# Kernel tuning notes

Hardware: AMD Instinct MI355X
Metric: run time of the kernel (lower is better)

Reference implementation:

```python
import jax, jax.numpy as jnp
import numpy as np

N_NODES = 100000
N_EDGES = 3200000
B = 64            # number of graphs / RNA batch
DIM = 16          # GINE hidden dim
NFP = 33          # protein node feature dim
EMB = 128         # embedding dim
MAXLEN = 3000     # rna_global length (conv1d in_channels)
LOCLEN = 2998     # rna_local length = 3000 - log4(64) + 1
NF = 32           # n_filters
KS = 8            # conv kernel size -> 128-8+1 = 121
FC_IN = NF * 121  # 3872
BN_EPS = 1e-5


def setup_inputs() -> dict:
    key = jax.random.key(0)
    ks = jax.random.split(key, 32)
    s = 0.1
    p = {}
    # forward data args
    p['pro_x'] = jax.random.normal(ks[0], (N_NODES, NFP), jnp.float32)
    p['pro_edge_index'] = jax.random.randint(ks[1], (2, N_EDGES), 0, N_NODES, jnp.int32)
    p['pro_weight'] = jax.random.uniform(ks[2], (N_EDGES, 1), jnp.float32)
    p['pro_batch'] = jnp.sort(jax.random.randint(ks[3], (N_NODES,), 0, B, jnp.int32))
    p['rna_global'] = jax.random.randint(ks[4], (B, MAXLEN), 0, 5, jnp.int32)
    p['rna_local'] = jax.random.randint(ks[5], (B, LOCLEN), 0, 65, jnp.int32)
    # GINE layer 1 (33 -> 16)
    p['g1_w1'] = jax.random.normal(ks[6], (NFP, DIM), jnp.float32) * s
    p['g1_b1'] = jnp.zeros((DIM,), jnp.float32)
    p['g1_w2'] = jax.random.normal(ks[7], (DIM, DIM), jnp.float32) * s
    p['g1_b2'] = jnp.zeros((DIM,), jnp.float32)
    p['g1_ew'] = jax.random.normal(ks[8], (1, NFP), jnp.float32) * s  # edge Linear(1, 33)
    p['g1_eb'] = jnp.zeros((NFP,), jnp.float32)
    p['g1_eps'] = jnp.zeros((), jnp.float32)
    # GINE layers 2-5 (16 -> 16), stacked on leading axis
    p['g_w1'] = jax.random.normal(ks[9], (4, DIM, DIM), jnp.float32) * s
    p['g_b1'] = jnp.zeros((4, DIM), jnp.float32)
    p['g_w2'] = jax.random.normal(ks[10], (4, DIM, DIM), jnp.float32) * s
    p['g_b2'] = jnp.zeros((4, DIM), jnp.float32)
    p['g_ew'] = jax.random.normal(ks[11], (4, 1, DIM), jnp.float32) * s  # edge Linear(1, 16)
    p['g_eb'] = jnp.zeros((4, DIM), jnp.float32)
    p['g_eps'] = jnp.zeros((4,), jnp.float32)
    # BatchNorm1d x5
    p['bn_gamma'] = jnp.ones((5, DIM), jnp.float32)
    p['bn_beta'] = jnp.zeros((5, DIM), jnp.float32)
    # fc1_xp (16 -> 128)
    p['fc1_xp_w'] = jax.random.normal(ks[12], (DIM, EMB), jnp.float32) * s
    p['fc1_xp_b'] = jnp.zeros((EMB,), jnp.float32)
    # RNA branch
    p['emb1'] = jax.random.normal(ks[13], (5, EMB), jnp.float32)
    p['emb2'] = jax.random.normal(ks[14], (65, EMB), jnp.float32)
    p['convr1_w'] = jax.random.normal(ks[15], (NF, MAXLEN, KS), jnp.float32) * 0.01
    p['convr1_b'] = jnp.zeros((NF,), jnp.float32)
    p['convr2_w'] = jax.random.normal(ks[16], (NF, LOCLEN, KS), jnp.float32) * 0.01
    p['convr2_b'] = jnp.zeros((NF,), jnp.float32)
    p['fcxr_w'] = jax.random.normal(ks[17], (FC_IN, EMB), jnp.float32) * 0.01
    p['fcxr_b'] = jnp.zeros((EMB,), jnp.float32)
    return p


def _gine(x, src, dst, ew, w1, b1, w2, b2, ew_w, ew_b, eps):
    # GINEConv: out = MLP((1+eps)*x + sum_j relu(x_j + edge_lin(e_ij)))
    e = ew @ ew_w + ew_b                       # [E, d]
    m = jax.nn.relu(x[src] + e)                # [E, d] gather + fuse
    agg = jax.ops.segment_sum(m, dst, num_segments=N_NODES)
    h = (1.0 + eps) * x + agg
    return jax.nn.relu(h @ w1 + b1) @ w2 + b2


def _bn(x, gamma, beta):
    mu = jnp.mean(x, axis=0)
    var = jnp.var(x, axis=0)
    return (x - mu) * jax.lax.rsqrt(var + BN_EPS) * gamma + beta


def _rna_branch(tokens, emb, cw, cb, fcw, fcb):
    x = emb[tokens]                            # [B, L, 128]
    y = jax.lax.conv_general_dilated(x, cw, (1,), 'VALID',
                                     dimension_numbers=('NCH', 'OIH', 'NCH'))
    y = y + cb[None, :, None]                  # [B, 32, 121]
    return y.reshape(y.shape[0], -1) @ fcw + fcb


def reference(pro_x, pro_edge_index, pro_weight, pro_batch, rna_global, rna_local,
              g1_w1, g1_b1, g1_w2, g1_b2, g1_ew, g1_eb, g1_eps,
              g_w1, g_b1, g_w2, g_b2, g_ew, g_eb, g_eps,
              bn_gamma, bn_beta, fc1_xp_w, fc1_xp_b,
              emb1, emb2, convr1_w, convr1_b, convr2_w, convr2_b, fcxr_w, fcxr_b):
    src, dst = pro_edge_index[0], pro_edge_index[1]
    # RNA global / local branches (shared fc_xr)
    xrg = _rna_branch(rna_global, emb1, convr1_w, convr1_b, fcxr_w, fcxr_b)
    xrl = _rna_branch(rna_local, emb2, convr2_w, convr2_b, fcxr_w, fcxr_b)
    # protein GINE stack
    xp = jax.nn.relu(_gine(pro_x, src, dst, pro_weight,
                           g1_w1, g1_b1, g1_w2, g1_b2, g1_ew, g1_eb, g1_eps))
    xp = _bn(xp, bn_gamma[0], bn_beta[0])
    for i in range(4):
        xp = jax.nn.relu(_gine(xp, src, dst, pro_weight,
                               g_w1[i], g_b1[i], g_w2[i], g_b2[i],
                               g_ew[i], g_eb[i], g_eps[i]))
        xp = _bn(xp, bn_gamma[i + 1], bn_beta[i + 1])
    # global mean pool over graphs
    sums = jax.ops.segment_sum(xp, pro_batch, num_segments=B)
    cnt = jax.ops.segment_sum(jnp.ones((N_NODES, 1), xp.dtype), pro_batch, num_segments=B)
    xp = jax.nn.relu((sums / jnp.maximum(cnt, 1.0)) @ fc1_xp_w + fc1_xp_b)
    # dropout in eval mode -> identity
    xc_rna = 0.5 * (xrg + xrl)
    return (xc_rna, xp)
```

## Files before the change

### kernel.cpp

```cpp
#include <hip/hip_runtime.h>
#include <hip/hip_fp16.h>

#define N_NODES 100000
#define N_EDGES 3200000
#define BGR 64
#define DIM 16
#define NFP 33
#define ROW1 32
#define H1STR 36
#define EMB 128
#define MAXLEN 3000
#define LOCLEN 2998
#define NF 32
#define KS 8
#define OUTT 121
#define FC_IN 3872
#define BN_EPSV 1e-5f
#define POOL_CHUNK 256
#define POOL_BLKS 391
#define MLPB 391
#define AGGB 3125
#define NBIN 391
#define BCNT_BLK 512
#define P1_CHUNK 4096
#define P1_BLOCKS 782
#define MAXBIN 9088
#define NKC 32
#define KCH 121
#define WDEC (1.f / 32767.f)

__global__ void __launch_bounds__(256) k_bincnt(const int* __restrict__ dst,
                                                int* __restrict__ bh) {
    __shared__ int hist[NBIN];
    int t = threadIdx.x, bid = blockIdx.x;
    for (int b = t; b < NBIN; b += 256) hist[b] = 0;
    __syncthreads();
    int e0 = bid * (N_EDGES / BCNT_BLK);
    int e1 = e0 + (N_EDGES / BCNT_BLK);
    for (int e = e0 + t; e < e1; e += 256) atomicAdd(&hist[dst[e] >> 8], 1);
    __syncthreads();
    for (int b = t; b < NBIN; b += 256) bh[b * BCNT_BLK + bid] = hist[b];
}

__global__ void __launch_bounds__(512) k_binscan(const int* __restrict__ bh,
                                                 int* __restrict__ binoff,
                                                 int* __restrict__ bincur) {
    __shared__ int sc[512];
    int t = threadIdx.x;
    int s = 0;
    if (t < NBIN) {
        const int* row = bh + t * BCNT_BLK;
        for (int k = 0; k < BCNT_BLK; k++) s += row[k];
    }
    sc[t] = s;
    __syncthreads();
    for (int off = 1; off < 512; off <<= 1) {
        int v = (t >= off) ? sc[t - off] : 0;
        __syncthreads();
        sc[t] += v;
        __syncthreads();
    }
    int excl = sc[t] - s;
    if (t <= NBIN) binoff[t] = excl;
    if (t < NBIN) bincur[t] = excl;
}

__global__ void __launch_bounds__(256) k_part1(const int* __restrict__ src,
                                               const int* __restrict__ dst,
                                               const float* __restrict__ w,
                                               int* __restrict__ bincur,
                                               int2* __restrict__ tmp_sw) {
    __shared__ int2 srec[P1_CHUNK];
    __shared__ unsigned short sbin[P1_CHUNK];
    __shared__ unsigned short sperm[P1_CHUNK];
    __shared__ int hist[NBIN];
    __shared__ int off[NBIN];
    __shared__ int cur[NBIN];
    __shared__ int base[NBIN];
    __shared__ int sc[512];
    int t = threadIdx.x;
    int g0 = blockIdx.x * P1_CHUNK;
    int cn = N_EDGES - g0; if (cn > P1_CHUNK) cn = P1_CHUNK;
    for (int b = t; b < NBIN; b += 256) hist[b] = 0;
    __syncthreads();
    for (int j = t; j < cn; j += 256) {
        int d = dst[g0 + j];
        int b = d >> 8;
        sbin[j] = (unsigned short)b;
        srec[j] = make_int2(src[g0 + j] | ((d & 255) << 20), __float_as_int(w[g0 + j]));
        atomicAdd(&hist[b], 1);
    }
    __syncthreads();
    sc[t] = (t < NBIN) ? hist[t] : 0;
    sc[256 + t] = (256 + t < NBIN) ? hist[256 + t] : 0;
    __syncthreads();
    for (int o = 1; o <= 256; o <<= 1) {
        int v0 = (t >= o) ? sc[t - o] : 0;
        int v1 = sc[256 + t - o];
        __syncthreads();
        sc[t] += v0;
        sc[256 + t] += v1;
        __syncthreads();
    }
    for (int b = t; b < NBIN; b += 256) {
        int e = sc[b] - hist[b];
        off[b] = e;
        cur[b] = e;
        int c = hist[b];
        base[b] = c ? atomicAdd(&bincur[b], c) : 0;
    }
    __syncthreads();
    for (int j = t; j < cn; j += 256) {
        int p = atomicAdd(&cur[sbin[j]], 1);
        sperm[p] = (unsigned short)j;
    }
    __syncthreads();
    for (int p = t; p < cn; p += 256) {
        int j = sperm[p];
        int b = sbin[j];
        tmp_sw[base[b] + (p - off[b])] = srec[j];
    }
}

__global__ void __launch_bounds__(256) k_part2(const int2* __restrict__ tmp_sw,
                                               const int* __restrict__ binoff,
                                               unsigned* __restrict__ er,
                                               int* __restrict__ ptr) {
    __shared__ unsigned char sdl[MAXBIN];
    __shared__ unsigned short perm[MAXBIN];
    __shared__ int hist[256];
    __shared__ int cur[256];
    __shared__ int sc[256];
    int t = threadIdx.x, b = blockIdx.x;
    int nlo = b << 8;
    int e0 = binoff[b], e1 = binoff[b + 1];
    int cnt = e1 - e0;
    int stage = cnt < MAXBIN ? cnt : MAXBIN;
    hist[t] = 0;
    __syncthreads();
    for (int j = t; j < stage; j += 256) {
        unsigned char dl = (unsigned char)((tmp_sw[e0 + j].x >> 20) & 255);
        sdl[j] = dl;
        atomicAdd(&hist[dl], 1);
    }
    for (int j = stage + t; j < cnt; j += 256)
        atomicAdd(&hist[(tmp_sw[e0 + j].x >> 20) & 255], 1);
    __syncthreads();
    int v = hist[t];
    sc[t] = v;
    __syncthreads();
    for (int off = 1; off < 256; off <<= 1) {
        int u = (t >= off) ? sc[t - off] : 0;
        __syncthreads();
        sc[t] += u;
        __syncthreads();
    }
    int excl = sc[t] - v;
    cur[t] = excl;
    if (nlo + t < N_NODES) ptr[nlo + t] = e0 + excl;
    if (b == NBIN - 1 && t == 0) ptr[N_NODES] = N_EDGES;
    __syncthreads();
    for (int j = t; j < stage; j += 256) {
        int p = atomicAdd(&cur[sdl[j]], 1);
        perm[p] = (unsigned short)j;
    }
    __syncthreads();
    for (int j = stage + t; j < cnt; j += 256) {
        int2 sw = tmp_sw[e0 + j];
        int p = atomicAdd(&cur[(sw.x >> 20) & 255], 1);
        unsigned wq = (unsigned)(__int_as_float(sw.y) * 32767.f + 0.5f);
        er[e0 + p] = ((unsigned)sw.x & 0x1FFFFu) | (wq << 17);
    }
    for (int p = t; p < stage; p += 256) {
        int2 sw = tmp_sw[e0 + perm[p]];
        unsigned wq = (unsigned)(__int_as_float(sw.y) * 32767.f + 0.5f);
        er[e0 + p] = ((unsigned)sw.x & 0x1FFFFu) | (wq << 17);
    }
}

__global__ void k_half1(const float* __restrict__ x, __half* __restrict__ xh,
                        __half* __restrict__ xh32) {
    int i = blockIdx.x * blockDim.x + threadIdx.x;
    if (i < N_NODES * NFP) {
        int n = i / NFP, f = i - n * NFP;
        __half v = __float2half(x[i]);
        if (f < 32) xh[n * ROW1 + f] = v;
        else xh32[n] = v;
    }
}

__device__ __forceinline__ void acc8p(float a[8], uint4 r, float wv,
                                      const float* __restrict__ ewf,
                                      const float* __restrict__ ebf) {
    float2 f01 = __half22float2(*(__half2*)&r.x);
    float2 f23 = __half22float2(*(__half2*)&r.y);
    float2 f45 = __half22float2(*(__half2*)&r.z);
    float2 f67 = __half22float2(*(__half2*)&r.w);
    float x[8] = {f01.x, f01.y, f23.x, f23.y, f45.x, f45.y, f67.x, f67.y};
    #pragma unroll
    for (int j = 0; j < 8; j++)
        a[j] += fmaxf(x[j] + fmaf(wv, ewf[j], ebf[j]), 0.f);
}

__device__ __forceinline__ void acc8s(float a[8], uint4 r, float wv,
                                      const float* __restrict__ scf,
                                      const float* __restrict__ cbf,
                                      const float* __restrict__ ewf) {
    float2 f01 = __half22float2(*(__half2*)&r.x);
    float2 f23 = __half22float2(*(__half2*)&r.y);
    float2 f45 = __half22float2(*(__half2*)&r.z);
    float2 f67 = __half22float2(*(__half2*)&r.w);
    float x[8] = {f01.x, f01.y, f23.x, f23.y, f45.x, f45.y, f67.x, f67.y};
    #pragma unroll
    for (int j = 0; j < 8; j++)
        a[j] += fmaxf(fmaf(x[j], scf[j], fmaf(wv, ewf[j], cbf[j])), 0.f);
}

__global__ void __launch_bounds__(256) k_agg1(
    const __half* __restrict__ xh, const __half* __restrict__ xh32,
    const int* __restrict__ ptr, const unsigned* __restrict__ er,
    const float* __restrict__ ew, const float* __restrict__ ebv,
    const float* __restrict__ epsp, float* __restrict__ h) {
    int t = threadIdx.x;
    int wave = t >> 6, lane = t & 63;
    int nl = lane >> 3;
    int slot = (lane >> 2) & 1;
    int q = lane & 3;
    float ewf[8], ebf[8];
    #pragma unroll
    for (int j = 0; j < 8; j++) { ewf[j] = ew[q * 8 + j]; ebf[j] = ebv[q * 8 + j]; }
    float ew32 = ew[32], eb32 = ebv[32];
    float ep = 1.f + epsp[0];
    int node = blockIdx.x * 32 + wave * 8 + nl;
    int e0 = ptr[node], e1 = ptr[node + 1];
    float a[8] = {0, 0, 0, 0, 0, 0, 0, 0};
    float a32 = 0.f;
    int i = e0 + slot;
    while (i + 2 < e1) {
        unsigned ev0 = er[i];
        unsigned ev1 = er[i + 2];
        int s0 = ev0 & 0x1FFFF, s1 = ev1 & 0x1FFFF;
        float wv0 = (float)(ev0 >> 17) * WDEC;
        float wv1 = (float)(ev1 >> 17) * WDEC;
        uint4 r0 = *(const uint4*)(xh + s0 * ROW1 + q * 8);
        uint4 r1 = *(const uint4*)(xh + s1 * ROW1 + q * 8);
        acc8p(a, r0, wv0, ewf, ebf);
        acc8p(a, r1, wv1, ewf, ebf);
        if (q == 0) {
            a32 += fmaxf(__half2float(xh32[s0]) + fmaf(wv0, ew32, eb32), 0.f);
            a32 += fmaxf(__half2float(xh32[s1]) + fmaf(wv1, ew32, eb32), 0.f);
        }
        i += 4;
    }
    if (i < e1) {
        unsigned ev = er[i];
        int s = ev & 0x1FFFF;
        float wv = (float)(ev >> 17) * WDEC;
        uint4 r = *(const uint4*)(xh + s * ROW1 + q * 8);
        acc8p(a, r, wv, ewf, ebf);
        if (q == 0)
            a32 += fmaxf(__half2float(xh32[s]) + fmaf(wv, ew32, eb32), 0.f);
    }
    #pragma unroll
    for (int j = 0; j < 8; j++) a[j] += __shfl_xor(a[j], 4);
    a32 += __shfl_xor(a32, 4);
    if (slot == 0) {
        uint4 sraw = *(const uint4*)(xh + node * ROW1 + q * 8);
        float2 s01 = __half22float2(*(__half2*)&sraw.x);
        float2 s23 = __half22float2(*(__half2*)&sraw.y);
        float2 s45 = __half22float2(*(__half2*)&sraw.z);
        float2 s67 = __half22float2(*(__half2*)&sraw.w);
        float* hp = h + node * H1STR + q * 8;
        *(float4*)hp = make_float4(ep * s01.x + a[0], ep * s01.y + a[1],
                                   ep * s23.x + a[2], ep * s23.y + a[3]);
        *(float4*)(hp + 4) = make_float4(ep * s45.x + a[4], ep * s45.y + a[5],
                                         ep * s67.x + a[6], ep * s67.y + a[7]);
        if (q == 0)
            h[node * H1STR + 32] = ep * __half2float(xh32[node]) + a32;
    }
}

__global__ void __launch_bounds__(256) k_agg16(
    const __half* __restrict__ zh, const int* __restrict__ ptr,
    const unsigned* __restrict__ er,
    const float* __restrict__ ew, const float* __restrict__ ebv,
    const float* __restrict__ epsp,
    const float* __restrict__ bnstat, const float* __restrict__ gamma,
    const float* __restrict__ beta, float* __restrict__ h) {
    int t = threadIdx.x;
    int wave = t >> 6, lane = t & 63;
    int nl = lane >> 3;
    int slot = (lane >> 1) & 3;
    int hh = lane & 1;
    float ep = 1.f + epsp[0];
    const float invn = 1.f / (float)N_NODES;
    float scf[8], shf[8], cbf[8], ewf[8];
    #pragma unroll
    for (int j = 0; j < 8; j++) {
        int f = hh * 8 + j;
        float mu = bnstat[f] * invn;
        float var = bnstat[DIM + f] * invn - mu * mu;
        float sc = gamma[f] * rsqrtf(var + BN_EPSV);
        scf[j] = sc;
        shf[j] = beta[f] - mu * sc;
        cbf[j] = shf[j] + ebv[f];
        ewf[j] = ew[f];
    }
    int node = blockIdx.x * 32 + wave * 8 + nl;
    int e0 = ptr[node], e1 = ptr[node + 1];
    float a[8] = {0, 0, 0, 0, 0, 0, 0, 0};
    int i = e0 + slot;
    while (i + 4 < e1) {
        unsigned ev0 = er[i];
        unsigned ev1 = er[i + 4];
        float wv0 = (float)(ev0 >> 17) * WDEC;
        float wv1 = (float)(ev1 >> 17) * WDEC;
        uint4 r0 = *(const uint4*)(zh + (ev0 & 0x1FFFFu) * DIM + hh * 8);
        uint4 r1 = *(const uint4*)(zh + (ev1 & 0x1FFFFu) * DIM + hh * 8);
        acc8s(a, r0, wv0, scf, cbf, ewf);
        acc8s(a, r1, wv1, scf, cbf, ewf);
        i += 8;
    }
    if (i < e1) {
        unsigned ev = er[i];
        float wv = (float)(ev >> 17) * WDEC;
        uint4 r = *(const uint4*)(zh + (ev & 0x1FFFFu) * DIM + hh * 8);
        acc8s(a, r, wv, scf, cbf, ewf);
    }
    #pragma unroll
    for (int j = 0; j < 8; j++) a[j] += __shfl_xor(a[j], 2);
    #pragma unroll
    for (int j = 0; j < 8; j++) a[j] += __shfl_xor(a[j], 4);
    if (slot == 0) {
        uint4 sraw = *(const uint4*)(zh + node * DIM + hh * 8);
        float2 s01 = __half22float2(*(__half2*)&sraw.x);
        float2 s23 = __half22float2(*(__half2*)&sraw.y);
        float2 s45 = __half22float2(*(__half2*)&sraw.z);
        float2 s67 = __half22float2(*(__half2*)&sraw.w);
        float xs[8] = {s01.x, s01.y, s23.x, s23.y, s45.x, s45.y, s67.x, s67.y};
        float o8[8];
        #pragma unroll
        for (int j = 0; j < 8; j++)
            o8[j] = ep * fmaf(xs[j], scf[j], shf[j]) + a[j];
        float* hp = h + node * DIM + hh * 8;
        *(float4*)hp = make_float4(o8[0], o8[1], o8[2], o8[3]);
        *(float4*)(hp + 4) = make_float4(o8[4], o8[5], o8[6], o8[7]);
    }
}

__device__ __forceinline__ void mlp_bn_tail(float zv[16], bool active, int t,
                                            float* __restrict__ part) {
    __shared__ float red[4][32];
    float zs[16], zq[16];
    #pragma unroll
    for (int o = 0; o < 16; o++) {
        zs[o] = active ? zv[o] : 0.f;
        zq[o] = active ? zv[o] * zv[o] : 0.f;
    }
    #pragma unroll
    for (int m = 1; m <= 32; m <<= 1) {
        #pragma unroll
        for (int o = 0; o < 16; o++) {
            zs[o] += __shfl_xor(zs[o], m);
            zq[o] += __shfl_xor(zq[o], m);
        }
    }
    int wave = t >> 6, lane = t & 63;
    if (lane == 0) {
        #pragma unroll
        for (int o = 0; o < 16; o++) {
            red[wave][o] = zs[o];
            red[wave][16 + o] = zq[o];
        }
    }
    __syncthreads();
    if (t < 32)
        part[blockIdx.x * 32 + t] = red[0][t] + red[1][t] + red[2][t] + red[3][t];
}

__device__ __forceinline__ void store_zh(__half* __restrict__ zh, int n, float zv[16]) {
    __half2 p[8];
    #pragma unroll
    for (int j = 0; j < 8; j++) p[j] = __floats2half2_rn(zv[2 * j], zv[2 * j + 1]);
    *(uint4*)(zh + n * DIM) = *(uint4*)&p[0];
    *(uint4*)(zh + n * DIM + 8) = *(uint4*)&p[4];
}

__global__ void __launch_bounds__(256) k_mlp16(
    const float* __restrict__ h,
    const float* __restrict__ W1, const float* __restrict__ b1,
    const float* __restrict__ W2, const float* __restrict__ b2,
    __half* __restrict__ zh, float* __restrict__ part) {
    __shared__ float W1s[256], W2s[256], b1s[16], b2s[16];
    int t = threadIdx.x;
    W1s[t] = W1[t];
    W2s[t] = W2[t];
    if (t < 16) { b1s[t] = b1[t]; b2s[t] = b2[t]; }
    __syncthreads();
    int n = blockIdx.x * 256 + t;
    bool active = n < N_NODES;
    float zv[16];
    if (active) {
        float hv[16];
        #pragma unroll
        for (int j = 0; j < 4; j++) {
            float4 v = *(const float4*)(h + n * DIM + j * 4);
            hv[j * 4] = v.x; hv[j * 4 + 1] = v.y; hv[j * 4 + 2] = v.z; hv[j * 4 + 3] = v.w;
        }
        float tv[16];
        #pragma unroll
        for (int o = 0; o < 16; o++) {
            float s = b1s[o];
            #pragma unroll
            for (int f = 0; f < 16; f++) s += hv[f] * W1s[f * 16 + o];
            tv[o] = fmaxf(s, 0.f);
        }
        #pragma unroll
        for (int o = 0; o < 16; o++) {
            float s = b2s[o];
            #pragma unroll
            for (int f = 0; f < 16; f++) s += tv[f] * W2s[f * 16 + o];
            zv[o] = fmaxf(s, 0.f);
        }
        store_zh(zh, n, zv);
    }
    mlp_bn_tail(zv, active, t, part);
}

__global__ void __launch_bounds__(256) k_mlp1(
    const float* __restrict__ h,
    const float* __restrict__ W1, const float* __restrict__ b1,
    const float* __restrict__ W2, const float* __restrict__ b2,
    __half* __restrict__ zh, float* __restrict__ part) {
    __shared__ float W1s[NFP * 16], W2s[256], b1s[16], b2s[16];
    int t = threadIdx.x;
    for (int j = t; j < NFP * 16; j += 256) W1s[j] = W1[j];
    W2s[t] = W2[t];
    if (t < 16) { b1s[t] = b1[t]; b2s[t] = b2[t]; }
    __syncthreads();
    int n = blockIdx.x * 256 + t;
    bool active = n < N_NODES;
    float zv[16];
    if (active) {
        float hv[NFP];
        #pragma unroll
        for (int j = 0; j < 8; j++) {
            float4 v = *(const float4*)(h + n * H1STR + j * 4);
            hv[j * 4] = v.x; hv[j * 4 + 1] = v.y; hv[j * 4 + 2] = v.z; hv[j * 4 + 3] = v.w;
        }
        hv[32] = h[n * H1STR + 32];
        float tv[16];
        #pragma unroll
        for (int o = 0; o < 16; o++) {
            float s = b1s[o];
            #pragma unroll
            for (int f = 0; f < NFP; f++) s += hv[f] * W1s[f * 16 + o];
            tv[o] = fmaxf(s, 0.f);
        }
        #pragma unroll
        for (int o = 0; o < 16; o++) {
            float s = b2s[o];
            #pragma unroll
            for (int f = 0; f < 16; f++) s += tv[f] * W2s[f * 16 + o];
            zv[o] = fmaxf(s, 0.f);
        }
        store_zh(zh, n, zv);
    }
    mlp_bn_tail(zv, active, t, part);
}

__global__ void __launch_bounds__(1024) k_bnred(const float* __restrict__ part,
                                                float* __restrict__ bnstat) {
    __shared__ float red[1024];
    int t = threadIdx.x;
    int f = t & 31, g = t >> 5;
    float s = 0.f;
    for (int i = g; i < MLPB; i += 32) s += part[i * 32 + f];
    red[t] = s;
    __syncthreads();
    for (int off = 512; off >= 32; off >>= 1) {
        if (t < off) red[t] += red[t + off];
        __syncthreads();
    }
    if (t < 32) bnstat[t] = red[t];
}

__global__ void __launch_bounds__(256) k_pool(const __half* __restrict__ zh,
                                              const int* __restrict__ batch,
                                              const float* __restrict__ bnstat,
                                              const float* __restrict__ gamma,
                                              const float* __restrict__ beta,
                                              float* __restrict__ gsum,
                                              float* __restrict__ gcnt) {
    __shared__ float lsum[BGR * DIM];
    __shared__ float lcnt[BGR];
    int t = threadIdx.x;
    for (int j = t; j < BGR * DIM; j += 256) lsum[j] = 0.f;
    if (t < BGR) lcnt[t] = 0.f;
    __syncthreads();
    int f = t & 15, r = t >> 4;
    const float invn = 1.f / (float)N_NODES;
    float mu = bnstat[f] * invn;
    float var = bnstat[DIM + f] * invn - mu * mu;
    float sc = gamma[f] * rsqrtf(var + BN_EPSV);
    float sh = beta[f] - mu * sc;
    int start = blockIdx.x * POOL_CHUNK;
    float acc = 0.f, cacc = 0.f;
    int cur = -1;
    for (int i = 0; i < POOL_CHUNK / 16; i++) {
        int n = start + r + i * 16;
        if (n >= N_NODES) break;
        int b = batch[n];
        if (b != cur) {
            if (cur >= 0) {
                atomicAdd(&lsum[cur * DIM + f], acc);
                if (f == 0) atomicAdd(&lcnt[cur], cacc);
            }
            cur = b; acc = 0.f; cacc = 0.f;
        }
        acc += fmaf(__half2float(zh[n * DIM + f]), sc, sh);
        cacc += 1.f;
    }
    if (cur >= 0) {
        atomicAdd(&lsum[cur * DIM + f], acc);
        if (f == 0) atomicAdd(&lcnt[cur], cacc);
    }
    __syncthreads();
    for (int j = t; j < BGR * DIM; j += 256) {
        float v = lsum[j];
        if (v != 0.f) atomicAdd(&gsum[j], v);
    }
    if (t < BGR) {
        float v = lcnt[t];
        if (v != 0.f) atomicAdd(&gcnt[t], v);
    }
}

__global__ void k_xp(const float* __restrict__ gsum, const float* __restrict__ gcnt,
                     const float* __restrict__ w, const float* __restrict__ bias,
                     float* __restrict__ out) {
    int b = blockIdx.x;
    int e = threadIdx.x;
    float inv = 1.f / fmaxf(gcnt[b], 1.f);
    float acc = bias[e];
    #pragma unroll
    for (int f = 0; f < DIM; f++) acc += gsum[b * DIM + f] * inv * w[f * EMB + e];
    out[b * EMB + e] = fmaxf(acc, 0.f);
}

__global__ void __launch_bounds__(256) k_bucket(const int* __restrict__ tok, int L, int V,
                                                int* __restrict__ blist,
                                                int* __restrict__ bptr) {
    __shared__ int hist[65];
    __shared__ int cursor[65];
    int b = blockIdx.x, t = threadIdx.x;
    if (t < V) hist[t] = 0;
    __syncthreads();
    for (int l = t; l < L; l += 256) atomicAdd(&hist[tok[b * L + l]], 1);
    __syncthreads();
    if (t == 0) {
        int run = 0;
        for (int v = 0; v < V; v++) {
            cursor[v] = run;
            bptr[b * (V + 1) + v] = run;
            run += hist[v];
        }
        bptr[b * (V + 1) + V] = run;
    }
    __syncthreads();
    for (int l = t; l < L; l += 256) {
        int v = tok[b * L + l];
        int p = atomicAdd(&cursor[v], 1);
        blist[b * L + p] = l;
    }
}

__global__ void __launch_bounds__(256) k_wsum(const int* __restrict__ blist,
                                              const int* __restrict__ bptr,
                                              const float* __restrict__ cw,
                                              float* __restrict__ W, int L, int V) {
    int b = blockIdx.x, v = blockIdx.y;
    int t = threadIdx.x, o = t >> 3, k = t & 7;
    int s = bptr[b * (V + 1) + v], e = bptr[b * (V + 1) + v + 1];
    __shared__ int tk[256];
    const float* cwp = cw + o * (L * KS) + k;
    float acc = 0.f;
    for (int j0 = s; j0 < e; j0 += 256) {
        int lim = e - j0; if (lim > 256) lim = 256;
        __syncthreads();
        if (t < lim) tk[t] = blist[b * L + j0 + t];
        __syncthreads();
        for (int j = 0; j < lim; j++) acc += cwp[tk[j] * KS];
    }
    W[((b * NF + o) * V + v) * KS + k] = acc;
}

__global__ void k_y(const float* __restrict__ Wg, const float* __restrict__ Wl,
                    const float* __restrict__ emb1, const float* __restrict__ emb2,
                    const float* __restrict__ cb1, const float* __restrict__ cb2,
                    float* __restrict__ yg, float* __restrict__ yl) {
    int which = blockIdx.y;
    int bo = blockIdx.x;
    int b = bo >> 5, o = bo & 31;
    int t = threadIdx.x;
    const float* W = which ? Wl : Wg;
    const float* emb = which ? emb2 : emb1;
    const float* cb = which ? cb2 : cb1;
    float* y = which ? yl : yg;
    int V = which ? 65 : 5;
    __shared__ float Wsh[65 * KS];
    const float* Wrow = W + (b * NF + o) * V * KS;
    for (int j = t; j < V * KS; j += 128) Wsh[j] = Wrow[j];
    __syncthreads();
    if (t < OUTT) {
        float acc = cb[o];
        for (int v = 0; v < V; v++) {
            const float* ep = emb + v * EMB + t;
            #pragma unroll
            for (int k = 0; k < KS; k++) acc += Wsh[v * KS + k] * ep[k];
        }
        y[(b * NF + o) * OUTT + t] = acc;
    }
}

__global__ void __launch_bounds__(128) k_fcpart(const float* __restrict__ yg,
                                                const float* __restrict__ yl,
                                                const float* __restrict__ w,
                                                float* __restrict__ partial) {
    int b = blockIdx.x, which = blockIdx.y, kc = blockIdx.z;
    const float* y = which ? yl : yg;
    int e = threadIdx.x;
    __shared__ float ych[KCH];
    int j0 = kc * KCH;
    if (e < KCH) ych[e] = y[b * FC_IN + j0 + e];
    __syncthreads();
    float acc = 0.f;
    #pragma unroll 4
    for (int jj = 0; jj < KCH; jj++) acc += ych[jj] * w[(j0 + jj) * EMB + e];
    partial[((which * BGR + b) * NKC + kc) * EMB + e] = acc;
}

__global__ void k_fcred(const float* __restrict__ partial, const float* __restrict__ bias,
                        float* __restrict__ out) {
    int b = blockIdx.x;
    int e = threadIdx.x;
    const float* pg = partial + b * NKC * EMB + e;
    const float* pl = partial + (BGR + b) * NKC * EMB + e;
    float ag = bias[e], al = bias[e];
    #pragma unroll
    for (int k = 0; k < NKC; k++) { ag += pg[k * EMB]; al += pl[k * EMB]; }
    out[b * EMB + e] = 0.5f * (ag + al);
}

extern "C" void kernel_launch(void* const* d_in, const int* in_sizes, int n_in,
                              void* d_out, int out_size, void* d_ws, size_t ws_size,
                              hipStream_t stream) {
    const float* pro_x = (const float*)d_in[0];
    const int* eidx = (const int*)d_in[1];
    const int* esrc = eidx;
    const int* edst = eidx + N_EDGES;
    const float* pw = (const float*)d_in[2];
    const int* batch = (const int*)d_in[3];
    const int* rg = (const int*)d_in[4];
    const int* rl = (const int*)d_in[5];
    const float* g1_w1 = (const float*)d_in[6];
    const float* g1_b1 = (const float*)d_in[7];
    const float* g1_w2 = (const float*)d_in[8];
    const float* g1_b2 = (const float*)d_in[9];
    const float* g1_ew = (const float*)d_in[10];
    const float* g1_eb = (const float*)d_in[11];
    const float* g1_eps = (const float*)d_in[12];
    const float* g_w1 = (const float*)d_in[13];
    const float* g_b1 = (const float*)d_in[14];
    const float* g_w2 = (const float*)d_in[15];
    const float* g_b2 = (const float*)d_in[16];
    const float* g_ew = (const float*)d_in[17];
    const float* g_eb = (const float*)d_in[18];
    const float* g_eps = (const float*)d_in[19];
    const float* bn_gamma = (const float*)d_in[20];
    const float* bn_beta = (const float*)d_in[21];
    const float* fc1_xp_w = (const float*)d_in[22];
    const float* fc1_xp_b = (const float*)d_in[23];
    const float* emb1 = (const float*)d_in[24];
    const float* emb2 = (const float*)d_in[25];
    const float* convr1_w = (const float*)d_in[26];
    const float* convr1_b = (const float*)d_in[27];
    const float* convr2_w = (const float*)d_in[28];
    const float* convr2_b = (const float*)d_in[29];
    const float* fcxr_w = (const float*)d_in[30];
    const float* fcxr_b = (const float*)d_in[31];
    float* out = (float*)d_out;

    float* wsf = (float*)d_ws;
    int* ptr       = (int*)wsf;        wsf += 100128;
    int* binoff    = (int*)wsf;        wsf += 512;
    int* bincur    = (int*)wsf;        wsf += 512;
    unsigned* er   = (unsigned*)wsf;   wsf += 2 * N_EDGES;
    float* stats   = wsf;              wsf += 1280;
    float* un = wsf;
    int2* tmp_sw          = (int2*)un;
    int* bh               = (int*)(un + 7200000);
    __half* zh   = (__half*)(un + 1600000);
    __half* xh1  = (__half*)(un + 2400000);
    __half* xh32 = (__half*)(un + 4000000);
    float* bpart = un + 4100000;
    float* Wg    = un + 4300000;
    float* Wl    = un + 4382000;
    float* yg    = un + 5447000;
    float* yl    = un + 5695000;
    int* blg     = (int*)(un + 5961000);
    int* bll     = (int*)(un + 6153000);
    int* bpg     = (int*)(un + 6345000);
    int* bpl     = (int*)(un + 6346000);
    float* fcpart = un + 6360000;
    float* h      = un + 7400000;
    float* gsum   = stats;
    float* gcnt   = stats + 1024;
    float* bnstat = stats + 1088;

    hipMemsetAsync(stats, 0, 1280 * sizeof(float), stream);

    k_bincnt<<<BCNT_BLK, 256, 0, stream>>>(edst, bh);
    k_binscan<<<1, 512, 0, stream>>>(bh, binoff, bincur);
    k_part1<<<P1_BLOCKS, 256, 0, stream>>>(esrc, edst, pw, bincur, tmp_sw);
    k_part2<<<NBIN, 256, 0, stream>>>(tmp_sw, binoff, er, ptr);

    k_half1<<<(N_NODES * NFP + 255) / 256, 256, 0, stream>>>(pro_x, xh1, xh32);

    k_bucket<<<BGR, 256, 0, stream>>>(rg, MAXLEN, 5, blg, bpg);
    k_bucket<<<BGR, 256, 0, stream>>>(rl, LOCLEN, 65, bll, bpl);
    k_wsum<<<dim3(BGR, 5), 256, 0, stream>>>(blg, bpg, convr1_w, Wg, MAXLEN, 5);
    k_wsum<<<dim3(BGR, 65), 256, 0, stream>>>(bll, bpl, convr2_w, Wl, LOCLEN, 65);
    k_y<<<dim3(BGR * NF, 2), 128, 0, stream>>>(Wg, Wl, emb1, emb2, convr1_b, convr2_b, yg, yl);
    k_fcpart<<<dim3(BGR, 2, NKC), 128, 0, stream>>>(yg, yl, fcxr_w, fcpart);
    k_fcred<<<BGR, 128, 0, stream>>>(fcpart, fcxr_b, out);

    k_agg1<<<AGGB, 256, 0, stream>>>(xh1, xh32, ptr, er, g1_ew, g1_eb, g1_eps, h);
    k_mlp1<<<MLPB, 256, 0, stream>>>(h, g1_w1, g1_b1, g1_w2, g1_b2, zh, bpart);
    k_bnred<<<1, 1024, 0, stream>>>(bpart, bnstat);
    for (int i = 0; i < 4; i++) {
        k_agg16<<<AGGB, 256, 0, stream>>>(zh, ptr, er,
                                          g_ew + i * DIM, g_eb + i * DIM, g_eps + i,
                                          bnstat + i * 32, bn_gamma + i * DIM,
                                          bn_beta + i * DIM, h);
        k_mlp16<<<MLPB, 256, 0, stream>>>(h, g_w1 + i * DIM * DIM, g_b1 + i * DIM,
                                          g_w2 + i * DIM * DIM, g_b2 + i * DIM, zh, bpart);
        k_bnred<<<1, 1024, 0, stream>>>(bpart, bnstat + (i + 1) * 32);
    }
    k_pool<<<POOL_BLKS, 256, 0, stream>>>(zh, batch, bnstat + 4 * 32,
                                          bn_gamma + 4 * DIM, bn_beta + 4 * DIM, gsum, gcnt);
    k_xp<<<BGR, EMB, 0, stream>>>(gsum, gcnt, fc1_xp_w, fc1_xp_b, out + BGR * EMB);
}
```

Measured before the change: 640.2 us.

## Drop per-node edge slot splitting in GINE aggregation, process more nodes per wave

The aggregation kernels previously split each node's edge list across 2 (agg1) or 4 (agg16) lane slots and merged the partial sums with shuffle reductions. Now each lane group owns one whole node and walks its edges serially with a 4-way unrolled gather, so each wave covers 2x or 4x more nodes and the grid shrinks accordingly. This removes the shuffle reductions and idle slot lanes, but lengthens per-lane serial chains and adds per-lane load imbalance from uneven degrees. In agg1, every lane of the quad now also loads the 33rd feature instead of only q==0.

```diff
diff --git a/kernel.cpp b/kernel.cpp
--- a/kernel.cpp
+++ b/kernel.cpp
@@ -19,7 +19,8 @@
 #define POOL_CHUNK 256
 #define POOL_BLKS 391
 #define MLPB 391
-#define AGGB 3125
+#define AGGB1 1563
+#define AGGB16 782
 #define NBIN 391
 #define BCNT_BLK 512
 #define P1_CHUNK 4096
@@ -223,48 +224,57 @@
     const float* __restrict__ epsp, float* __restrict__ h) {
     int t = threadIdx.x;
     int wave = t >> 6, lane = t & 63;
-    int nl = lane >> 3;
-    int slot = (lane >> 2) & 1;
+    int nl = lane >> 2;
     int q = lane & 3;
     float ewf[8], ebf[8];
     #pragma unroll
     for (int j = 0; j < 8; j++) { ewf[j] = ew[q * 8 + j]; ebf[j] = ebv[q * 8 + j]; }
     float ew32 = ew[32], eb32 = ebv[32];
     float ep = 1.f + epsp[0];
-    int node = blockIdx.x * 32 + wave * 8 + nl;
-    int e0 = ptr[node], e1 = ptr[node + 1];
+    int node = blockIdx.x * 64 + wave * 16 + nl;
+    bool act = node < N_NODES;
+    int e0 = 0, e1 = 0;
+    if (act) { e0 = ptr[node]; e1 = ptr[node + 1]; }
     float a[8] = {0, 0, 0, 0, 0, 0, 0, 0};
     float a32 = 0.f;
-    int i = e0 + slot;
-    while (i + 2 < e1) {
-        unsigned ev0 = er[i];
-        unsigned ev1 = er[i + 2];
+    int i = e0;
+    while (i + 3 < e1) {
+        unsigned ev0 = er[i], ev1 = er[i + 1], ev2 = er[i + 2], ev3 = er[i + 3];
         int s0 = ev0 & 0x1FFFF, s1 = ev1 & 0x1FFFF;
+        int s2 = ev2 & 0x1FFFF, s3 = ev3 & 0x1FFFF;
         float wv0 = (float)(ev0 >> 17) * WDEC;
         float wv1 = (float)(ev1 >> 17) * WDEC;
+        float wv2 = (float)(ev2 >> 17) * WDEC;
+        float wv3 = (float)(ev3 >> 17) * WDEC;
         uint4 r0 = *(const uint4*)(xh + s0 * ROW1 + q * 8);
         uint4 r1 = *(const uint4*)(xh + s1 * ROW1 + q * 8);
+        uint4 r2 = *(const uint4*)(xh + s2 * ROW1 + q * 8);
+        uint4 r3 = *(const uint4*)(xh + s3 * ROW1 + q * 8);
+        float x0 = __half2float(xh32[s0]);
+        float x1 = __half2float(xh32[s1]);
+        float x2 = __half2float(xh32[s2]);
+        float x3 = __half2float(xh32[s3]);
         acc8p(a, r0, wv0, ewf, ebf);
         acc8p(a, r1, wv1, ewf, ebf);
-        if (q == 0) {
-            a32 += fmaxf(__half2float(xh32[s0]) + fmaf(wv0, ew32, eb32), 0.f);
-            a32 += fmaxf(__half2float(xh32[s1]) + fmaf(wv1, ew32, eb32), 0.f);
-        }
+        acc8p(a, r2, wv2, ewf, ebf);
+        acc8p(a, r3, wv3, ewf, ebf);
+        a32 += fmaxf(x0 + fmaf(wv0, ew32, eb32), 0.f);
+        a32 += fmaxf(x1 + fmaf(wv1, ew32, eb32), 0.f);
+        a32 += fmaxf(x2 + fmaf(wv2, ew32, eb32), 0.f);
+        a32 += fmaxf(x3 + fmaf(wv3, ew32, eb32), 0.f);
         i += 4;
     }
-    if (i < e1) {
+    while (i < e1) {
         unsigned ev = er[i];
         int s = ev & 0x1FFFF;
         float wv = (float)(ev >> 17) * WDEC;
         uint4 r = *(const uint4*)(xh + s * ROW1 + q * 8);
+        float xs = __half2float(xh32[s]);
         acc8p(a, r, wv, ewf, ebf);
-        if (q == 0)
-            a32 += fmaxf(__half2float(xh32[s]) + fmaf(wv, ew32, eb32), 0.f);
-    }
-    #pragma unroll
-    for (int j = 0; j < 8; j++) a[j] += __shfl_xor(a[j], 4);
-    a32 += __shfl_xor(a32, 4);
-    if (slot == 0) {
+        a32 += fmaxf(xs + fmaf(wv, ew32, eb32), 0.f);
+        i++;
+    }
+    if (act) {
         uint4 sraw = *(const uint4*)(xh + node * ROW1 + q * 8);
         float2 s01 = __half22float2(*(__half2*)&sraw.x);
         float2 s23 = __half22float2(*(__half2*)&sraw.y);
@@ -289,12 +299,11 @@
     const float* __restrict__ beta, float* __restrict__ h) {
     int t = threadIdx.x;
     int wave = t >> 6, lane = t & 63;
-    int nl = lane >> 3;
-    int slot = (lane >> 1) & 3;
+    int nl = lane >> 1;
     int hh = lane & 1;
     float ep = 1.f + epsp[0];
     const float invn = 1.f / (float)N_NODES;
-    float scf[8], shf[8], cbf[8], ewf[8];
+    float scf[8], cbf[8], ewf[8];
     #pragma unroll
     for (int j = 0; j < 8; j++) {
         int f = hh * 8 + j;
@@ -302,36 +311,39 @@
         float var = bnstat[DIM + f] * invn - mu * mu;
         float sc = gamma[f] * rsqrtf(var + BN_EPSV);
         scf[j] = sc;
-        shf[j] = beta[f] - mu * sc;
-        cbf[j] = shf[j] + ebv[f];
+        cbf[j] = (beta[f] - mu * sc) + ebv[f];
         ewf[j] = ew[f];
     }
-    int node = blockIdx.x * 32 + wave * 8 + nl;
-    int e0 = ptr[node], e1 = ptr[node + 1];
+    int node = blockIdx.x * 128 + wave * 32 + nl;
+    bool act = node < N_NODES;
+    int e0 = 0, e1 = 0;
+    if (act) { e0 = ptr[node]; e1 = ptr[node + 1]; }
     float a[8] = {0, 0, 0, 0, 0, 0, 0, 0};
-    int i = e0 + slot;
-    while (i + 4 < e1) {
-        unsigned ev0 = er[i];
-        unsigned ev1 = er[i + 4];
+    int i = e0;
+    while (i + 3 < e1) {
+        unsigned ev0 = er[i], ev1 = er[i + 1], ev2 = er[i + 2], ev3 = er[i + 3];
         float wv0 = (float)(ev0 >> 17) * WDEC;
         float wv1 = (float)(ev1 >> 17) * WDEC;
+        float wv2 = (float)(ev2 >> 17) * WDEC;
+        float wv3 = (float)(ev3 >> 17) * WDEC;
         uint4 r0 = *(const uint4*)(zh + (ev0 & 0x1FFFFu) * DIM + hh * 8);
         uint4 r1 = *(const uint4*)(zh + (ev1 & 0x1FFFFu) * DIM + hh * 8);
+        uint4 r2 = *(const uint4*)(zh + (ev2 & 0x1FFFFu) * DIM + hh * 8);
+        uint4 r3 = *(const uint4*)(zh + (ev3 & 0x1FFFFu) * DIM + hh * 8);
         acc8s(a, r0, wv0, scf, cbf, ewf);
         acc8s(a, r1, wv1, scf, cbf, ewf);
-        i += 8;
-    }
-    if (i < e1) {
+        acc8s(a, r2, wv2, scf, cbf, ewf);
+        acc8s(a, r3, wv3, scf, cbf, ewf);
+        i += 4;
+    }
+    while (i < e1) {
         unsigned ev = er[i];
         float wv = (float)(ev >> 17) * WDEC;
         uint4 r = *(const uint4*)(zh + (ev & 0x1FFFFu) * DIM + hh * 8);
         acc8s(a, r, wv, scf, cbf, ewf);
-    }
-    #pragma unroll
-    for (int j = 0; j < 8; j++) a[j] += __shfl_xor(a[j], 2);
-    #pragma unroll
-    for (int j = 0; j < 8; j++) a[j] += __shfl_xor(a[j], 4);
-    if (slot == 0) {
+        i++;
+    }
+    if (act) {
         uint4 sraw = *(const uint4*)(zh + node * DIM + hh * 8);
         float2 s01 = __half22float2(*(__half2*)&sraw.x);
         float2 s23 = __half22float2(*(__half2*)&sraw.y);
@@ -340,8 +352,10 @@
         float xs[8] = {s01.x, s01.y, s23.x, s23.y, s45.x, s45.y, s67.x, s67.y};
         float o8[8];
         #pragma unroll
-        for (int j = 0; j < 8; j++)
-            o8[j] = ep * fmaf(xs[j], scf[j], shf[j]) + a[j];
+        for (int j = 0; j < 8; j++) {
+            float shf = cbf[j] - ebv[hh * 8 + j];
+            o8[j] = ep * fmaf(xs[j], scf[j], shf) + a[j];
+        }
         float* hp = h + node * DIM + hh * 8;
         *(float4*)hp = make_float4(o8[0], o8[1], o8[2], o8[3]);
         *(float4*)(hp + 4) = make_float4(o8[4], o8[5], o8[6], o8[7]);
@@ -735,14 +749,14 @@
     k_fcpart<<<dim3(BGR, 2, NKC), 128, 0, stream>>>(yg, yl, fcxr_w, fcpart);
     k_fcred<<<BGR, 128, 0, stream>>>(fcpart, fcxr_b, out);
 
-    k_agg1<<<AGGB, 256, 0, stream>>>(xh1, xh32, ptr, er, g1_ew, g1_eb, g1_eps, h);
+    k_agg1<<<AGGB1, 256, 0, stream>>>(xh1, xh32, ptr, er, g1_ew, g1_eb, g1_eps, h);
     k_mlp1<<<MLPB, 256, 0, stream>>>(h, g1_w1, g1_b1, g1_w2, g1_b2, zh, bpart);
     k_bnred<<<1, 1024, 0, stream>>>(bpart, bnstat);
     for (int i = 0; i < 4; i++) {
-        k_agg16<<<AGGB, 256, 0, stream>>>(zh, ptr, er,
-                                          g_ew + i * DIM, g_eb + i * DIM, g_eps + i,
-                                          bnstat + i * 32, bn_gamma + i * DIM,
-                                          bn_beta + i * DIM, h);
+        k_agg16<<<AGGB16, 256, 0, stream>>>(zh, ptr, er,
+                                            g_ew + i * DIM, g_eb + i * DIM, g_eps + i,
+                                            bnstat + i * 32, bn_gamma + i * DIM,
+                                            bn_beta + i * DIM, h);
         k_mlp16<<<MLPB, 256, 0, stream>>>(h, g_w1 + i * DIM * DIM, g_b1 + i * DIM,
                                           g_w2 + i * DIM * DIM, g_b2 + i * DIM, zh, bpart);
         k_bnred<<<1, 1024, 0, stream>>>(bpart, bnstat + (i + 1) * 32);
```

New measurement: 688.1 us. 1.07x slower.
